# Performance work log

Hardware: AMD Instinct MI355X
Metric: run time of the kernel (lower is better)

## Reference

```python
import jax, jax.numpy as jnp
import numpy as np

B, C_IN, C_KEY, C_VAL, C_OUT = 1, 64, 32, 64, 64
H = W = D = 64
SCALE = 8


def setup_inputs() -> dict:
    key = jax.random.key(0)
    ks = jax.random.split(key, 4)
    init = lambda k, shape, fan: jax.random.normal(k, shape, jnp.float32) * (fan ** -0.5)
    return {
        "x": jax.random.normal(ks[0], (B, C_IN, H, W, D), jnp.float32),
        "w_key": init(ks[1], (C_KEY, C_IN), C_IN),
        "b_key": jnp.zeros((C_KEY,), jnp.float32),
        "w_value": init(ks[2], (C_VAL, C_IN), C_IN),
        "b_value": jnp.zeros((C_VAL,), jnp.float32),
        "w_out": init(ks[3], (C_OUT, C_VAL), C_VAL),
        "b_out": jnp.zeros((C_OUT,), jnp.float32),
        "scale": SCALE,
    }


def _proj(t, wgt, bias):
    # 1x1x1 Conv3d == pointwise channel matmul
    return jnp.einsum('bchwd,oc->bohwd', t, wgt) + bias[None, :, None, None, None]


def _windows(t, s):
    # [B,C,H,W,D] -> [B, s^3 windows, hb*wb*db tokens, C]
    b, c, h, w, d = t.shape
    hb, wb, db = h // s, w // s, d // s
    t = t.reshape(b, c, s, hb, s, wb, s, db)
    t = t.transpose(0, 2, 4, 6, 3, 5, 7, 1)
    return t.reshape(b, s * s * s, hb * wb * db, c), (hb, wb, db)


def _unwindows(t, s, blk):
    hb, wb, db = blk
    b, c = t.shape[0], t.shape[-1]
    t = t.reshape(b, s, s, s, hb, wb, db, c)
    t = t.transpose(0, 7, 1, 4, 2, 5, 3, 6)
    return t.reshape(b, c, s * hb, s * wb, s * db)


def reference(x, w_key, b_key, w_value, b_value, w_out, b_out, scale):
    # f_query = f_key (shared module in the original)
    k_full = _proj(x, w_key, b_key)
    v_full = _proj(x, w_value, b_value)
    qw, blk = _windows(k_full, scale)
    kw = qw  # shared projection -> query == key
    vw, _ = _windows(v_full, scale)
    sim = jnp.einsum('bnlc,bnmc->bnlm', qw, kw) * (qw.shape[-1] ** -0.5)
    sim = jax.nn.softmax(sim, axis=-1)
    ctx = jnp.einsum('bnlm,bnmc->bnlc', sim, vw)
    ctx = _unwindows(ctx, scale, blk)
    return _proj(ctx, w_out, b_out)
```

## Files before the change

kernel.cpp:

```cpp
#include <hip/hip_runtime.h>

typedef unsigned short u16;
typedef __bf16 bf16x8 __attribute__((ext_vector_type(8)));
typedef float f32x16 __attribute__((ext_vector_type(16)));

union B8 { bf16x8 v; u16 s[8]; unsigned u[4]; uint4 u4; };

__device__ __forceinline__ unsigned cvtpk(float a, float b) {
    unsigned r;
    asm("v_cvt_pk_bf16_f32 %0, %1, %2" : "=v"(r) : "v"(a), "v"(b));
    return r;
}
__device__ __forceinline__ float ex2(float x) { return __builtin_amdgcn_exp2f(x); }
__device__ __forceinline__ float ex2p(float x) {
    float n = floorf(x);
    float f = x - n;
    float p = fmaf(f, 0.0802449f, 0.224368f);
    p = fmaf(f, p, 0.695348f);
    p = fmaf(f, p, 1.0f);
    int e = ((int)n + 127) << 23;
    return __int_as_float(e) * p;
}
__device__ __forceinline__ void swap32(unsigned &a, unsigned &b) {
    asm("v_permlane32_swap_b32 %0, %1" : "+v"(a), "+v"(b));
}
__device__ __forceinline__ B8 load_w8(const float* __restrict__ p, float s) {
    float4 lo = ((const float4*)p)[0];
    float4 hi = ((const float4*)p)[1];
    B8 r;
    r.u[0] = cvtpk(lo.x * s, lo.y * s);
    r.u[1] = cvtpk(lo.z * s, lo.w * s);
    r.u[2] = cvtpk(hi.x * s, hi.y * s);
    r.u[3] = cvtpk(hi.z * s, hi.w * s);
    return r;
}
__device__ __forceinline__ f32x16 mfma32(const B8 a, const B8 b, f32x16 c) {
    return __builtin_amdgcn_mfma_f32_32x32x16_bf16(a.v, b.v, c, 0, 0, 0);
}
__device__ __forceinline__ int kidx(int row, int sl) {
    return row * 32 + (((sl ^ (row >> 1)) & 3) << 3);
}
__device__ __forceinline__ void build_b(const float* p, B8& b0, B8& b1) {
    unsigned c0 = cvtpk(p[0], p[1]),   c1 = cvtpk(p[2], p[3]);
    unsigned c2 = cvtpk(p[4], p[5]),   c3 = cvtpk(p[6], p[7]);
    unsigned c4 = cvtpk(p[8], p[9]),   c5 = cvtpk(p[10], p[11]);
    unsigned c6 = cvtpk(p[12], p[13]), c7 = cvtpk(p[14], p[15]);
    swap32(c0, c2); swap32(c1, c3); swap32(c4, c6); swap32(c5, c7);
    b0.u[0] = c0; b0.u[1] = c1; b0.u[2] = c2; b0.u[3] = c3;
    b1.u[0] = c4; b1.u[1] = c5; b1.u[2] = c6; b1.u[3] = c7;
}

#define VOFF 16384
#define XOFF 49664
#define NSM  68096

__global__ __launch_bounds__(512, 1)
void psab_fused(const float* __restrict__ x,
                const float* __restrict__ wk, const float* __restrict__ bk,
                const float* __restrict__ wv, const float* __restrict__ bv,
                const float* __restrict__ wo, const float* __restrict__ bo,
                float* __restrict__ out)
{
    __shared__ __align__(16) u16 smem[NSM];
    const int t    = threadIdx.x;
    const int lane = t & 63;
    const int wid  = t >> 6;
    const int cl   = lane & 31;
    const int h5   = lane >> 5;

    const int bid = blockIdx.x;
    const int n   = (bid & 7) * 64 + (bid >> 3);
    const int sh = n >> 6, sw = (n >> 3) & 7, sd = n & 7;
    const size_t base_vox = (size_t)(sh * 8) * 4096 + (size_t)(sw * 8) * 64 + (size_t)(sd * 8);

    const float WSC = 0.50506330f;

    B8 wkA[4], wvB[2][4];
#pragma unroll
    for (int kc = 0; kc < 4; ++kc)
        wkA[kc] = load_w8(wk + cl * 64 + kc * 16 + h5 * 8, WSC);
#pragma unroll
    for (int nb = 0; nb < 2; ++nb)
#pragma unroll
        for (int kc = 0; kc < 4; ++kc)
            wvB[nb][kc] = load_w8(wv + (nb * 32 + cl) * 64 + kc * 16 + h5 * 8, 1.0f);
    float bkv[16];
#pragma unroll
    for (int r = 0; r < 16; ++r)
        bkv[r] = bk[(r & 3) + 8 * (r >> 2) + 4 * h5] * WSC;
    const float vbias[2] = { bv[cl], bv[32 + cl] };

    const f32x16 z16 = {0,0,0,0,0,0,0,0,0,0,0,0,0,0,0,0};

    const int cS = t & 63;
    const int r2 = t >> 6;
    float4 L4[4], H4[4];
#define LDX(cc)                                                                              \
    _Pragma("unroll")                                                                        \
    for (int i = 0; i < 4; ++i) {                                                            \
        const float* gp = x + (size_t)cS * 262144 + base_vox + ((cc) * 4 + i) * 4096 + r2 * 64; \
        L4[i] = ((const float4*)gp)[0];                                                      \
        H4[i] = ((const float4*)gp)[1];                                                      \
    }
#define STX()                                                                                \
    _Pragma("unroll")                                                                        \
    for (int i = 0; i < 4; ++i) {                                                            \
        unsigned a0 = cvtpk(L4[i].x, L4[i].y), a1 = cvtpk(L4[i].z, L4[i].w);                 \
        unsigned a2 = cvtpk(H4[i].x, H4[i].y), a3 = cvtpk(H4[i].z, H4[i].w);                 \
        u16* xp = &smem[XOFF + (i * 64 + r2 * 8) * 72 + cS];                                 \
        xp[0 * 72] = (u16)a0; xp[1 * 72] = (u16)(a0 >> 16);                                  \
        xp[2 * 72] = (u16)a1; xp[3 * 72] = (u16)(a1 >> 16);                                  \
        xp[4 * 72] = (u16)a2; xp[5 * 72] = (u16)(a2 >> 16);                                  \
        xp[6 * 72] = (u16)a3; xp[7 * 72] = (u16)(a3 >> 16);                                  \
    }

    LDX(0)
    STX()
    __syncthreads();
    LDX(1)

#pragma unroll
    for (int cc = 0; cc < 2; ++cc) {
        const int tokb = cc * 256 + wid * 32;
        B8 ax[4];
#pragma unroll
        for (int kc = 0; kc < 4; ++kc)
            ax[kc].u4 = *(const uint4*)&smem[XOFF + (wid * 32 + cl) * 72 + kc * 16 + h5 * 8];
        f32x16 kd = mfma32(wkA[0], ax[0], z16);
        kd = mfma32(wkA[1], ax[1], kd);
        kd = mfma32(wkA[2], ax[2], kd);
        kd = mfma32(wkA[3], ax[3], kd);
        const int trow = tokb + cl;
#pragma unroll
        for (int g = 0; g < 4; ++g) {
            uint2 pk;
            pk.x = cvtpk(kd[4 * g + 0] + bkv[4 * g + 0], kd[4 * g + 1] + bkv[4 * g + 1]);
            pk.y = cvtpk(kd[4 * g + 2] + bkv[4 * g + 2], kd[4 * g + 3] + bkv[4 * g + 3]);
            *(uint2*)&smem[kidx(trow, g) + 4 * h5] = pk;
        }
#pragma unroll
        for (int nb = 0; nb < 2; ++nb) {
            f32x16 vd = mfma32(ax[0], wvB[nb][0], z16);
            vd = mfma32(ax[1], wvB[nb][1], vd);
            vd = mfma32(ax[2], wvB[nb][2], vd);
            vd = mfma32(ax[3], wvB[nb][3], vd);
            const int cv = nb * 32 + cl;
            const float vb = vbias[nb];
#pragma unroll
            for (int rq = 0; rq < 4; ++rq) {
                uint2 pk;
                pk.x = cvtpk(vd[rq * 4 + 0] + vb, vd[rq * 4 + 1] + vb);
                pk.y = cvtpk(vd[rq * 4 + 2] + vb, vd[rq * 4 + 3] + vb);
                *(uint2*)&smem[VOFF + cv * 520 + tokb + rq * 8 + 4 * h5] = pk;
            }
        }
        if (cc == 0) {
            __syncthreads();
            STX()
            __syncthreads();
        }
    }
    __syncthreads();

    B8 qB[2][2];
#pragma unroll
    for (int qb = 0; qb < 2; ++qb)
#pragma unroll
        for (int kc = 0; kc < 2; ++kc)
            qB[qb][kc].u4 = *(const uint4*)&smem[kidx(wid * 64 + qb * 32 + cl, 2 * kc + h5)];

    B8 ones;
    ones.u[0] = 0x3f803f80u; ones.u[1] = 0x3f803f80u;
    ones.u[2] = 0x3f803f80u; ones.u[3] = 0x3f803f80u;

    f32x16 ctx00 = z16, ctx01 = z16, ctx10 = z16, ctx11 = z16;
    f32x16 lacc0 = z16, lacc1 = z16;

#define SM(sv, lac, c0, c1)                                                                   \
    {                                                                                         \
        float p[16];                                                                          \
        _Pragma("unroll")                                                                     \
        for (int i2 = 0; i2 < 13; ++i2) p[i2] = ex2(sv[i2]);                                  \
        p[13] = ex2p(sv[13]); p[14] = ex2p(sv[14]); p[15] = ex2p(sv[15]);                     \
        B8 pb0, pb1;                                                                          \
        build_b(p, pb0, pb1);                                                                 \
        __builtin_amdgcn_s_setprio(1);                                                        \
        lac = mfma32(ones, pb0, lac);                                                         \
        lac = mfma32(ones, pb1, lac);                                                         \
        c0 = mfma32(va00, pb0, c0);                                                           \
        c0 = mfma32(va01, pb1, c0);                                                           \
        c1 = mfma32(va10, pb0, c1);                                                           \
        c1 = mfma32(va11, pb1, c1);                                                           \
        __builtin_amdgcn_s_setprio(0);                                                        \
    }

#pragma unroll 1
    for (int ci = 0; ci < 16; ++ci) {
        const int m0 = ci * 32;
        B8 kA0, kA1, va00, va01, va10, va11;
        kA0.u4  = *(const uint4*)&smem[kidx(m0 + cl, h5)];
        kA1.u4  = *(const uint4*)&smem[kidx(m0 + cl, 2 + h5)];
        va00.u4 = *(const uint4*)&smem[VOFF + cl * 520 + m0 + h5 * 8];
        va01.u4 = *(const uint4*)&smem[VOFF + cl * 520 + m0 + 16 + h5 * 8];
        va10.u4 = *(const uint4*)&smem[VOFF + (32 + cl) * 520 + m0 + h5 * 8];
        va11.u4 = *(const uint4*)&smem[VOFF + (32 + cl) * 520 + m0 + 16 + h5 * 8];

        __builtin_amdgcn_s_setprio(1);
        f32x16 s0 = mfma32(kA0, qB[0][0], z16); s0 = mfma32(kA1, qB[0][1], s0);
        f32x16 s1 = mfma32(kA0, qB[1][0], z16); s1 = mfma32(kA1, qB[1][1], s1);
        __builtin_amdgcn_s_setprio(0);

        SM(s0, lacc0, ctx00, ctx01)
        SM(s1, lacc1, ctx10, ctx11)
    }

    const float inv0 = 1.0f / lacc0[0];
    const float inv1 = 1.0f / lacc1[0];

    B8 aw[2][4];
#pragma unroll
    for (int cob = 0; cob < 2; ++cob)
#pragma unroll
        for (int kc = 0; kc < 4; ++kc)
            aw[cob][kc] = load_w8(wo + (cob * 32 + cl) * 64 + kc * 16 + h5 * 8, 1.0f);

    float pn[16];
    B8 cq0[4], cq1[4];
#pragma unroll
    for (int i = 0; i < 16; ++i) pn[i] = ctx00[i] * inv0;
    build_b(pn, cq0[0], cq0[1]);
#pragma unroll
    for (int i = 0; i < 16; ++i) pn[i] = ctx01[i] * inv0;
    build_b(pn, cq0[2], cq0[3]);
#pragma unroll
    for (int i = 0; i < 16; ++i) pn[i] = ctx10[i] * inv1;
    build_b(pn, cq1[0], cq1[1]);
#pragma unroll
    for (int i = 0; i < 16; ++i) pn[i] = ctx11[i] * inv1;
    build_b(pn, cq1[2], cq1[3]);

    __syncthreads();

    float* fout = (float*)((char*)smem + wid * 16384);
#pragma unroll
    for (int cob = 0; cob < 2; ++cob) {
        f32x16 od0 = mfma32(aw[cob][0], cq0[0], z16);
        od0 = mfma32(aw[cob][1], cq0[1], od0);
        od0 = mfma32(aw[cob][2], cq0[2], od0);
        od0 = mfma32(aw[cob][3], cq0[3], od0);
        f32x16 od1 = mfma32(aw[cob][0], cq1[0], z16);
        od1 = mfma32(aw[cob][1], cq1[1], od1);
        od1 = mfma32(aw[cob][2], cq1[2], od1);
        od1 = mfma32(aw[cob][3], cq1[3], od1);
#pragma unroll
        for (int r = 0; r < 16; ++r) {
            const int row = cob * 32 + (r & 3) + 8 * (r >> 2) + 4 * h5;
            fout[row * 64 + cl]      = od0[r];
            fout[row * 64 + 32 + cl] = od1[r];
        }
    }

    float* outw = out + base_vox + (size_t)wid * 4096;
    const int lq = lane >> 4, lr = lane & 15;
#pragma unroll
    for (int it = 0; it < 16; ++it) {
        const int co = it * 4 + lq;
        float4 v4 = *(const float4*)&fout[co * 64 + lr * 4];
        const float bco = bo[co];
        v4.x += bco; v4.y += bco; v4.z += bco; v4.w += bco;
        const int wb = lr >> 1, db0 = (lr & 1) * 4;
        *(float4*)&outw[(size_t)co * 262144 + wb * 64 + db0] = v4;
    }
}

extern "C" void kernel_launch(void* const* d_in, const int* in_sizes, int n_in,
                              void* d_out, int out_size, void* d_ws, size_t ws_size,
                              hipStream_t stream) {
    const float* x  = (const float*)d_in[0];
    const float* wk = (const float*)d_in[1];
    const float* bk = (const float*)d_in[2];
    const float* wv = (const float*)d_in[3];
    const float* bv = (const float*)d_in[4];
    const float* wo = (const float*)d_in[5];
    const float* bo = (const float*)d_in[6];
    float* o = (float*)d_out;
    psab_fused<<<dim3(512), dim3(512), 0, stream>>>(x, wk, bk, wv, bv, wo, bo, o);
}
```

Before: 76.05 us.

## Double-buffer K/V fragment loads, fold output bias into MFMA, store directly

The attention inner loop is unrolled by two with ping-pong register fragments, so the LDS reads for the next 32-key chunk are issued while the current chunk is being computed. The s_setprio hints are dropped, and the polynomial exp2 emulation on three lanes is replaced by the hardware exp2 for all sixteen values. The epilogue no longer stages the output tile in shared memory behind a barrier. Instead the bias is added through an extra MFMA against a constant vector and the results are written straight to global memory as scalar stores, which removes the LDS round-trip but gives up coalesced float4 stores and rounds the bias to bf16.

```diff
diff --git a/kernel.cpp b/kernel.cpp
--- a/kernel.cpp
+++ b/kernel.cpp
@@ -12,15 +12,6 @@
     return r;
 }
 __device__ __forceinline__ float ex2(float x) { return __builtin_amdgcn_exp2f(x); }
-__device__ __forceinline__ float ex2p(float x) {
-    float n = floorf(x);
-    float f = x - n;
-    float p = fmaf(f, 0.0802449f, 0.224368f);
-    p = fmaf(f, p, 0.695348f);
-    p = fmaf(f, p, 1.0f);
-    int e = ((int)n + 127) << 23;
-    return __int_as_float(e) * p;
-}
 __device__ __forceinline__ void swap32(unsigned &a, unsigned &b) {
     asm("v_permlane32_swap_b32 %0, %1" : "+v"(a), "+v"(b));
 }
@@ -176,42 +167,50 @@
     f32x16 ctx00 = z16, ctx01 = z16, ctx10 = z16, ctx11 = z16;
     f32x16 lacc0 = z16, lacc1 = z16;
 
-#define SM(sv, lac, c0, c1)                                                                   \
+#define LOADF(P, M0)                                                                          \
+    P##k0.u4  = *(const uint4*)&smem[kidx((M0) + cl, h5)];                                    \
+    P##k1.u4  = *(const uint4*)&smem[kidx((M0) + cl, 2 + h5)];                                \
+    P##v00.u4 = *(const uint4*)&smem[VOFF + cl * 520 + (M0) + h5 * 8];                        \
+    P##v01.u4 = *(const uint4*)&smem[VOFF + cl * 520 + (M0) + 16 + h5 * 8];                   \
+    P##v10.u4 = *(const uint4*)&smem[VOFF + (32 + cl) * 520 + (M0) + h5 * 8];                 \
+    P##v11.u4 = *(const uint4*)&smem[VOFF + (32 + cl) * 520 + (M0) + 16 + h5 * 8];
+
+#define SM(sv, lac, c0, c1, P)                                                                \
     {                                                                                         \
         float p[16];                                                                          \
         _Pragma("unroll")                                                                     \
-        for (int i2 = 0; i2 < 13; ++i2) p[i2] = ex2(sv[i2]);                                  \
-        p[13] = ex2p(sv[13]); p[14] = ex2p(sv[14]); p[15] = ex2p(sv[15]);                     \
+        for (int i2 = 0; i2 < 16; ++i2) p[i2] = ex2(sv[i2]);                                  \
         B8 pb0, pb1;                                                                          \
         build_b(p, pb0, pb1);                                                                 \
-        __builtin_amdgcn_s_setprio(1);                                                        \
         lac = mfma32(ones, pb0, lac);                                                         \
         lac = mfma32(ones, pb1, lac);                                                         \
-        c0 = mfma32(va00, pb0, c0);                                                           \
-        c0 = mfma32(va01, pb1, c0);                                                           \
-        c1 = mfma32(va10, pb0, c1);                                                           \
-        c1 = mfma32(va11, pb1, c1);                                                           \
-        __builtin_amdgcn_s_setprio(0);                                                        \
-    }
-
+        c0 = mfma32(P##v00, pb0, c0);                                                         \
+        c0 = mfma32(P##v01, pb1, c0);                                                         \
+        c1 = mfma32(P##v10, pb0, c1);                                                         \
+        c1 = mfma32(P##v11, pb1, c1);                                                         \
+    }
+
+#define COMPUTE(P)                                                                            \
+    {                                                                                         \
+        f32x16 s0 = mfma32(P##k0, qB[0][0], z16); s0 = mfma32(P##k1, qB[0][1], s0);           \
+        f32x16 s1 = mfma32(P##k0, qB[1][0], z16); s1 = mfma32(P##k1, qB[1][1], s1);           \
+        SM(s0, lacc0, ctx00, ctx01, P)                                                        \
+        SM(s1, lacc1, ctx10, ctx11, P)                                                        \
+    }
+
+    B8 fAk0, fAk1, fAv00, fAv01, fAv10, fAv11;
+    B8 fBk0, fBk1, fBv00, fBv01, fBv10, fBv11;
+    LOADF(fA, 0)
 #pragma unroll 1
-    for (int ci = 0; ci < 16; ++ci) {
-        const int m0 = ci * 32;
-        B8 kA0, kA1, va00, va01, va10, va11;
-        kA0.u4  = *(const uint4*)&smem[kidx(m0 + cl, h5)];
-        kA1.u4  = *(const uint4*)&smem[kidx(m0 + cl, 2 + h5)];
-        va00.u4 = *(const uint4*)&smem[VOFF + cl * 520 + m0 + h5 * 8];
-        va01.u4 = *(const uint4*)&smem[VOFF + cl * 520 + m0 + 16 + h5 * 8];
-        va10.u4 = *(const uint4*)&smem[VOFF + (32 + cl) * 520 + m0 + h5 * 8];
-        va11.u4 = *(const uint4*)&smem[VOFF + (32 + cl) * 520 + m0 + 16 + h5 * 8];
-
-        __builtin_amdgcn_s_setprio(1);
-        f32x16 s0 = mfma32(kA0, qB[0][0], z16); s0 = mfma32(kA1, qB[0][1], s0);
-        f32x16 s1 = mfma32(kA0, qB[1][0], z16); s1 = mfma32(kA1, qB[1][1], s1);
-        __builtin_amdgcn_s_setprio(0);
-
-        SM(s0, lacc0, ctx00, ctx01)
-        SM(s1, lacc1, ctx10, ctx11)
+    for (int cp = 0; cp < 8; ++cp) {
+        const int m1 = cp * 64 + 32;
+        LOADF(fB, m1)
+        COMPUTE(fA)
+        if (cp < 7) {
+            const int m2 = cp * 64 + 64;
+            LOADF(fA, m2)
+        }
+        COMPUTE(fB)
     }
 
     const float inv0 = 1.0f / lacc0[0];
@@ -239,37 +238,36 @@
     for (int i = 0; i < 16; ++i) pn[i] = ctx11[i] * inv1;
     build_b(pn, cq1[2], cq1[3]);
 
-    __syncthreads();
-
-    float* fout = (float*)((char*)smem + wid * 16384);
+    B8 abo[2], ones16;
+    {
+        unsigned b0 = cvtpk(bo[cl], bo[cl]);
+        unsigned b1 = cvtpk(bo[32 + cl], bo[32 + cl]);
+        abo[0].u[0] = b0; abo[0].u[1] = b0; abo[0].u[2] = b0; abo[0].u[3] = b0;
+        abo[1].u[0] = b1; abo[1].u[1] = b1; abo[1].u[2] = b1; abo[1].u[3] = b1;
+        ones16.u[0] = 0x3d803d80u; ones16.u[1] = 0x3d803d80u;
+        ones16.u[2] = 0x3d803d80u; ones16.u[3] = 0x3d803d80u;
+    }
+
+    float* ob = out + base_vox;
+    const int voxb = wid * 4096 + (cl >> 3) * 64 + (cl & 7) + h5 * 1048576;
 #pragma unroll
     for (int cob = 0; cob < 2; ++cob) {
         f32x16 od0 = mfma32(aw[cob][0], cq0[0], z16);
         od0 = mfma32(aw[cob][1], cq0[1], od0);
         od0 = mfma32(aw[cob][2], cq0[2], od0);
         od0 = mfma32(aw[cob][3], cq0[3], od0);
+        od0 = mfma32(abo[cob], ones16, od0);
         f32x16 od1 = mfma32(aw[cob][0], cq1[0], z16);
         od1 = mfma32(aw[cob][1], cq1[1], od1);
         od1 = mfma32(aw[cob][2], cq1[2], od1);
         od1 = mfma32(aw[cob][3], cq1[3], od1);
+        od1 = mfma32(abo[cob], ones16, od1);
 #pragma unroll
         for (int r = 0; r < 16; ++r) {
-            const int row = cob * 32 + (r & 3) + 8 * (r >> 2) + 4 * h5;
-            fout[row * 64 + cl]      = od0[r];
-            fout[row * 64 + 32 + cl] = od1[r];
-        }
-    }
-
-    float* outw = out + base_vox + (size_t)wid * 4096;
-    const int lq = lane >> 4, lr = lane & 15;
-#pragma unroll
-    for (int it = 0; it < 16; ++it) {
-        const int co = it * 4 + lq;
-        float4 v4 = *(const float4*)&fout[co * 64 + lr * 4];
-        const float bco = bo[co];
-        v4.x += bco; v4.y += bco; v4.z += bco; v4.w += bco;
-        const int wb = lr >> 1, db0 = (lr & 1) * 4;
-        *(float4*)&outw[(size_t)co * 262144 + wb * 64 + db0] = v4;
+            const int cop = cob * 32 + (r & 3) + 8 * (r >> 2);
+            ob[(size_t)cop * 262144 + voxb]       = od0[r];
+            ob[(size_t)cop * 262144 + voxb + 256] = od1[r];
+        }
     }
 }
 
```

New measurement: 68.87 us (median of 2 runs). 9.4% less time.
